# Optimization experiments

Measured on AMD Instinct MI355X. Metric: run time of the kernel, lower is better.

Reference implementation:

```python
import jax, jax.numpy as jnp
import numpy as np

N, E = 25000, 400000
NIN, NOUT, HID = 32, 32, 128


def setup_inputs() -> dict:
    key = jax.random.key(0)
    ks = jax.random.split(key, 8)
    s = lambda d: 1.0 / np.sqrt(d)
    return {
        "x": jax.random.normal(ks[0], (N, NIN), jnp.float32),
        "edge_index": jax.random.randint(ks[1], (2, E), 0, N, jnp.int64),
        "edge_attr": jax.random.normal(ks[2], (E, NIN), jnp.float32),
        # edge-MLP: Linear(NIN,HID) -> ReLU -> Linear(HID, NIN*NOUT)
        "w1": jax.random.normal(ks[3], (NIN, HID), jnp.float32) * s(NIN),
        "b1": jnp.zeros((HID,), jnp.float32),
        "w2": jax.random.normal(ks[4], (HID, NIN * NOUT), jnp.float32) * s(HID),
        "b2": jnp.zeros((NIN * NOUT,), jnp.float32),
        # NNConv root weight and bias
        "root": jax.random.normal(ks[5], (NIN, NOUT), jnp.float32) * s(NIN),
        "bias": jnp.zeros((NOUT,), jnp.float32),
    }


def reference(x, edge_index, edge_attr, w1, b1, w2, b2, root, bias):
    src, dst = edge_index[0], edge_index[1]
    # per-edge weight matrices from edge-attr MLP: [E, NIN, NOUT]
    h = jax.nn.relu(edge_attr @ w1 + b1)
    W = (h @ w2 + b2).reshape(-1, NIN, NOUT)
    # gather source features, per-edge small matmul: [E, NOUT]
    msg = jnp.einsum("ei,eio->eo", x[src], W)
    # scatter-add to target nodes (PyG default aggr='add')
    agg = jax.ops.segment_sum(msg, dst, num_segments=N)
    # root/self transform + bias
    return agg + x @ root + bias
```

## Files before the change

kernel.cpp:

```cpp
#include <hip/hip_runtime.h>
#include <hip/hip_fp16.h>


#define NN 25000
#define EE 400000

typedef _Float16 f16x8 __attribute__((ext_vector_type(8)));
typedef float    f32x16 __attribute__((ext_vector_type(16)));

__global__ __launch_bounds__(256) void prep_kernel(
    const float* __restrict__ w1, const float* __restrict__ w2,
    const float* __restrict__ b2,
    _Float16* __restrict__ w2p, _Float16* __restrict__ w1p, _Float16* __restrict__ b2p,
    float4* __restrict__ part4, int nzero4)
{
    int b = blockIdx.x;
    if (b < 532) {
        int t = b * 256 + threadIdx.x;
        if (t < 131072) {
            int j = t & 7, lane = (t >> 3) & 63, ih = (t >> 9) & 1, c = t >> 10;
            w2p[t] = (_Float16)w2[c * 1024 + (ih * 16 + ((lane >> 5) << 3) + j) * 32 + (lane & 31)];
        } else if (t < 135168) {
            int u = t - 131072;
            int j = u & 7, lane = (u >> 3) & 63, kk = (u >> 9) & 1, r = u >> 10;
            w1p[u] = (_Float16)w1[(kk * 16 + ((lane >> 5) << 3) + j) * 128 + r * 32 + (lane & 31)];
        } else {
            int u = t - 135168;
            int j = u & 7, lane = (u >> 3) & 63, ih = u >> 9;
            b2p[u] = (_Float16)b2[(ih * 16 + ((lane >> 5) << 3) + j) * 32 + (lane & 31)];
        }
    } else {
        int z = (b - 532) * 256 + threadIdx.x;
        if (z < nzero4) part4[z] = make_float4(0.f, 0.f, 0.f, 0.f);
    }
}

__global__ __launch_bounds__(256) void final_kernel(
    const float* __restrict__ x, const float* __restrict__ root,
    const float* __restrict__ bias, const float* __restrict__ part,
    int ncopies, float* __restrict__ out)
{
    int gid = blockIdx.x * 256 + threadIdx.x;
    int n = gid >> 5, o = gid & 31;
    float acc = bias[o];
    const float* xr = x + (n << 5);
#pragma unroll
    for (int i = 0; i < 32; ++i)
        acc = fmaf(xr[i], root[(i << 5) + o], acc);
    for (int c = 0; c < ncopies; ++c) acc += part[(size_t)c * 800000 + gid];
    out[gid] = acc;
}

__global__ __launch_bounds__(128, 2) void edge_kernel(
    const float*    __restrict__ x,
    const int*      __restrict__ ei,
    const float*    __restrict__ ea,
    const float*    __restrict__ b1,
    const _Float16* __restrict__ w2p,
    const _Float16* __restrict__ w1p,
    const _Float16* __restrict__ b2p,
    float* __restrict__ outp, int copyMask)
{
    __shared__ unsigned short hTq[2][32][32][4];

    const int t    = threadIdx.x;
    const int w    = t >> 6;
    const int lane = t & 63;
    const int l    = lane & 31;
    const int half = lane >> 5;

    const int  ebraw = blockIdx.x * 256 + w * 128;
    const bool live  = (ebraw + 128) <= EE;
    const int  ebw   = live ? ebraw : (EE - 128);

    float* __restrict__ myout = outp + (size_t)(blockIdx.x & copyMask) * 800000;

    union u8h { f16x8 v; __half2 h2[4]; };

    const f16x8* __restrict__ w2f = (const f16x8*)w2p;

    f16x8 BA[2], BB[2], BC[2], BD[2];
    auto loadCol = [&](int j, f16x8 (&B)[2]) {
        const f16x8* p = w2f + (size_t)j * 128 + lane;
        B[0] = p[0];
        B[1] = p[64];
    };
    loadCol(0, BA);
    loadCol(1, BB);
    loadCol(2, BC);
    loadCol(3, BD);

    u8h eaf[4][2];
#pragma unroll
    for (int g = 0; g < 4; ++g)
#pragma unroll
        for (int kk = 0; kk < 2; ++kk) {
            const float* p = ea + (size_t)(ebw + g * 32 + l) * 32 + kk * 16 + half * 8;
            float4 a0 = *(const float4*)p;
            float4 a1 = *(const float4*)(p + 4);
            eaf[g][kk].h2[0] = __float22half2_rn(make_float2(a0.x, a0.y));
            eaf[g][kk].h2[1] = __float22half2_rn(make_float2(a0.z, a0.w));
            eaf[g][kk].h2[2] = __float22half2_rn(make_float2(a1.x, a1.y));
            eaf[g][kk].h2[3] = __float22half2_rn(make_float2(a1.z, a1.w));
        }

    __half2 xs[4][8];
#pragma unroll
    for (int g = 0; g < 4; ++g) {
        int s = ei[ebw + g * 32 + l];
#pragma unroll
        for (int ih = 0; ih < 2; ++ih) {
            float4 a0 = *(const float4*)(x + s * 32 + ih * 16 + half * 8);
            float4 a1 = *(const float4*)(x + s * 32 + ih * 16 + half * 8 + 4);
            xs[g][ih*4+0] = __float22half2_rn(make_float2(a0.x, a0.y));
            xs[g][ih*4+1] = __float22half2_rn(make_float2(a0.z, a0.w));
            xs[g][ih*4+2] = __float22half2_rn(make_float2(a1.x, a1.y));
            xs[g][ih*4+3] = __float22half2_rn(make_float2(a1.z, a1.w));
        }
    }

    f32x16 acc[4];
#pragma unroll
    for (int g = 0; g < 4; ++g)
#pragma unroll
        for (int i = 0; i < 16; ++i) acc[g][i] = 0.f;

    auto phase1 = [&](int r) {
        f16x8 w1f0 = *(const f16x8*)(w1p + ((r * 2 + 0) * 64 + lane) * 8);
        f16x8 w1f1 = *(const f16x8*)(w1p + ((r * 2 + 1) * 64 + lane) * 8);
#pragma unroll
        for (int g = 0; g < 4; ++g) {
            f32x16 h;
#pragma unroll
            for (int i = 0; i < 16; ++i) h[i] = 0.f;
            h = __builtin_amdgcn_mfma_f32_32x32x16_f16(w1f0, eaf[g][0].v, h, 0, 0, 0);
            h = __builtin_amdgcn_mfma_f32_32x32x16_f16(w1f1, eaf[g][1].v, h, 0, 0, 0);
#pragma unroll
            for (int i = 0; i < 16; ++i) {
                int row = (i & 3) + ((i >> 2) << 3) + (half << 2);
                float hv = fmaxf(h[i] + b1[r * 32 + row], 0.f);
                hTq[w][row][l][g] = __half_as_ushort(__float2half(hv));
            }
        }
    };

    auto computeCol = [&](int cs, const f16x8 (&B)[2]) {
        uint2 u = *(const uint2*)&hTq[w][cs][l][0];
        __half2 ha = *reinterpret_cast<const __half2*>(&u.x);
        __half2 hb = *reinterpret_cast<const __half2*>(&u.y);
        __half2 d[4];
        d[0] = __half2half2(__low2half(ha));
        d[1] = __half2half2(__high2half(ha));
        d[2] = __half2half2(__low2half(hb));
        d[3] = __half2half2(__high2half(hb));
#pragma unroll
        for (int ih = 0; ih < 2; ++ih) {
            f16x8 bfr = B[ih];
#pragma unroll
            for (int g = 0; g < 4; ++g) {
                u8h A;
#pragma unroll
                for (int p = 0; p < 4; ++p)
                    A.h2[p] = __hmul2(d[g], xs[g][ih * 4 + p]);
                acc[g] = __builtin_amdgcn_mfma_f32_32x32x16_f16(A.v, bfr, acc[g], 0, 0, 0);
            }
        }
    };

#pragma unroll 1
    for (int r = 0; r < 4; ++r) {
        phase1(r);
#pragma unroll 1
        for (int q = 0; q < 8; ++q) {
            const int j = r * 32 + q * 4;
            computeCol(q * 4 + 0, BA); loadCol(j + 4, BA);
            computeCol(q * 4 + 1, BB); loadCol(j + 5, BB);
            computeCol(q * 4 + 2, BC); loadCol(j + 6, BC);
            computeCol(q * 4 + 3, BD); loadCol(j + 7, BD);
        }
    }

#pragma unroll
    for (int ih = 0; ih < 2; ++ih) {
        f16x8 bfr = *(const f16x8*)(b2p + (ih * 64 + lane) * 8);
#pragma unroll
        for (int g = 0; g < 4; ++g) {
            u8h A;
#pragma unroll
            for (int p = 0; p < 4; ++p) A.h2[p] = xs[g][ih * 4 + p];
            acc[g] = __builtin_amdgcn_mfma_f32_32x32x16_f16(A.v, bfr, acc[g], 0, 0, 0);
        }
    }

    if (live) {
#pragma unroll
        for (int g = 0; g < 4; ++g)
#pragma unroll
            for (int i = 0; i < 16; ++i) {
                int el = (i & 3) + ((i >> 2) << 3) + (half << 2);
                atomicAdd(myout + ei[EE + ebw + g * 32 + el] * 32 + l, acc[g][i]);
            }
    }
}

extern "C" void kernel_launch(void* const* d_in, const int* in_sizes, int n_in,
                              void* d_out, int out_size, void* d_ws, size_t ws_size,
                              hipStream_t stream) {
    const float* x    = (const float*)d_in[0];
    const int*   ei   = (const int*)  d_in[1];
    const float* ea   = (const float*)d_in[2];
    const float* w1   = (const float*)d_in[3];
    const float* b1   = (const float*)d_in[4];
    const float* w2   = (const float*)d_in[5];
    const float* b2   = (const float*)d_in[6];
    const float* root = (const float*)d_in[7];
    const float* bias = (const float*)d_in[8];
    float* out = (float*)d_out;

    _Float16* w2p = (_Float16*)d_ws;
    _Float16* w1p = (_Float16*)((char*)d_ws + 262144);
    _Float16* b2p = (_Float16*)((char*)d_ws + 270336);
    const size_t partOff = 272384;
    const size_t one = 800000ull * sizeof(float);
    size_t avail = (ws_size > partOff) ? ws_size - partOff : 0;
    int nc = 0;
    for (int c = 8; c >= 1; c >>= 1)
        if ((size_t)c * one <= avail) { nc = c; break; }

    float* part = (float*)((char*)d_ws + partOff);
    if (nc > 0) {
        int nzero4 = nc * 200000;
        int zb = (nzero4 + 255) / 256;
        prep_kernel<<<532 + zb, 256, 0, stream>>>(w1, w2, b2, w2p, w1p, b2p,
                                                  (float4*)part, nzero4);
        edge_kernel<<<(EE + 255) / 256, 128, 0, stream>>>(x, ei, ea, b1, w2p, w1p, b2p,
                                                          part, nc - 1);
        final_kernel<<<(NN * 32) / 256, 256, 0, stream>>>(x, root, bias, part, nc, out);
    } else {
        prep_kernel<<<532, 256, 0, stream>>>(w1, w2, b2, w2p, w1p, b2p, (float4*)part, 0);
        final_kernel<<<(NN * 32) / 256, 256, 0, stream>>>(x, root, bias, part, 0, out);
        edge_kernel<<<(EE + 255) / 256, 128, 0, stream>>>(x, ei, ea, b1, w2p, w1p, b2p,
                                                          out, 0);
    }
}
```

Baseline: 235.7 us.

## Replace atomic scatter with CSR build and gather-based aggregation

```diff
diff --git a/kernel.cpp b/kernel.cpp
--- a/kernel.cpp
+++ b/kernel.cpp
@@ -12,7 +12,7 @@
     const float* __restrict__ w1, const float* __restrict__ w2,
     const float* __restrict__ b2,
     _Float16* __restrict__ w2p, _Float16* __restrict__ w1p, _Float16* __restrict__ b2p,
-    float4* __restrict__ part4, int nzero4)
+    float4* __restrict__ zero4, int nzero4)
 {
     int b = blockIdx.x;
     if (b < 532) {
@@ -31,8 +31,73 @@
         }
     } else {
         int z = (b - 532) * 256 + threadIdx.x;
-        if (z < nzero4) part4[z] = make_float4(0.f, 0.f, 0.f, 0.f);
-    }
+        if (z < nzero4) zero4[z] = make_float4(0.f, 0.f, 0.f, 0.f);
+    }
+}
+
+__global__ __launch_bounds__(256) void hist_kernel(const int* __restrict__ ei,
+                                                   int* __restrict__ deg)
+{
+    int e = blockIdx.x * 256 + threadIdx.x;
+    if (e < EE) atomicAdd(&deg[ei[EE + e]], 1);
+}
+
+__global__ __launch_bounds__(1024) void scan_kernel(const int* __restrict__ deg,
+                                                    int* __restrict__ rowptr,
+                                                    int* __restrict__ cur)
+{
+    __shared__ int part[1024];
+    const int t = threadIdx.x;
+    const int base = t * 25;
+    const int cnt = (base < NN) ? ((NN - base < 25) ? (NN - base) : 25) : 0;
+    int s = 0;
+    for (int k = 0; k < cnt; ++k) s += deg[base + k];
+    part[t] = s;
+    __syncthreads();
+    for (int off = 1; off < 1024; off <<= 1) {
+        int v = (t >= off) ? part[t - off] : 0;
+        __syncthreads();
+        part[t] += v;
+        __syncthreads();
+    }
+    int excl = (t == 0) ? 0 : part[t - 1];
+    for (int k = 0; k < cnt; ++k) {
+        int d = deg[base + k];
+        rowptr[base + k] = excl;
+        cur[base + k]    = excl;
+        excl += d;
+    }
+    if (t == 1023) rowptr[NN] = part[1023];
+}
+
+__global__ __launch_bounds__(256) void fill_kernel(const int* __restrict__ ei,
+                                                   int* __restrict__ cur,
+                                                   int* __restrict__ eidx)
+{
+    int e = blockIdx.x * 256 + threadIdx.x;
+    if (e < EE) {
+        int pos = atomicAdd(&cur[ei[EE + e]], 1);
+        eidx[pos] = e;
+    }
+}
+
+__global__ __launch_bounds__(256) void final_gather(
+    const float* __restrict__ x, const float* __restrict__ root,
+    const float* __restrict__ bias, const float* __restrict__ msg,
+    const int* __restrict__ rowptr, const int* __restrict__ eidx,
+    float* __restrict__ out)
+{
+    int gid = blockIdx.x * 256 + threadIdx.x;
+    int n = gid >> 5, o = gid & 31;
+    float acc = bias[o];
+    const float* xr = x + (n << 5);
+#pragma unroll
+    for (int i = 0; i < 32; ++i)
+        acc = fmaf(xr[i], root[(i << 5) + o], acc);
+    int k0 = rowptr[n], k1 = rowptr[n + 1];
+    for (int k = k0; k < k1; ++k)
+        acc += msg[(size_t)eidx[k] * 32 + o];
+    out[gid] = acc;
 }
 
 __global__ __launch_bounds__(256) void final_kernel(
@@ -59,7 +124,7 @@
     const _Float16* __restrict__ w2p,
     const _Float16* __restrict__ w1p,
     const _Float16* __restrict__ b2p,
-    float* __restrict__ outp, int copyMask)
+    float* __restrict__ outp, int copyMask, int useStore)
 {
     __shared__ unsigned short hTq[2][32][32][4];
 
@@ -193,13 +258,23 @@
     }
 
     if (live) {
-#pragma unroll
-        for (int g = 0; g < 4; ++g)
-#pragma unroll
-            for (int i = 0; i < 16; ++i) {
-                int el = (i & 3) + ((i >> 2) << 3) + (half << 2);
-                atomicAdd(myout + ei[EE + ebw + g * 32 + el] * 32 + l, acc[g][i]);
-            }
+        if (useStore) {
+#pragma unroll
+            for (int g = 0; g < 4; ++g)
+#pragma unroll
+                for (int i = 0; i < 16; ++i) {
+                    int el = (i & 3) + ((i >> 2) << 3) + (half << 2);
+                    myout[(size_t)(ebw + g * 32 + el) * 32 + l] = acc[g][i];
+                }
+        } else {
+#pragma unroll
+            for (int g = 0; g < 4; ++g)
+#pragma unroll
+                for (int i = 0; i < 16; ++i) {
+                    int el = (i & 3) + ((i >> 2) << 3) + (half << 2);
+                    atomicAdd(myout + ei[EE + ebw + g * 32 + el] * 32 + l, acc[g][i]);
+                }
+        }
     }
 }
 
@@ -220,6 +295,35 @@
     _Float16* w2p = (_Float16*)d_ws;
     _Float16* w1p = (_Float16*)((char*)d_ws + 262144);
     _Float16* b2p = (_Float16*)((char*)d_ws + 270336);
+
+    const size_t degOff  = 272384;
+    const size_t rowOff  = 372384;
+    const size_t curOff  = 472400;
+    const size_t eidxOff = 572400;
+    const size_t msgOff  = 2172400;
+    const size_t needStore = msgOff + (size_t)EE * 32 * 4;
+
+    if (ws_size >= needStore) {
+        int*   deg    = (int*)((char*)d_ws + degOff);
+        int*   rowptr = (int*)((char*)d_ws + rowOff);
+        int*   cur    = (int*)((char*)d_ws + curOff);
+        int*   eidx   = (int*)((char*)d_ws + eidxOff);
+        float* msg    = (float*)((char*)d_ws + msgOff);
+
+        int nzero4 = 25000 / 4;
+        int zb = (nzero4 + 255) / 256;
+        prep_kernel<<<532 + zb, 256, 0, stream>>>(w1, w2, b2, w2p, w1p, b2p,
+                                                  (float4*)deg, nzero4);
+        hist_kernel<<<(EE + 255) / 256, 256, 0, stream>>>(ei, deg);
+        scan_kernel<<<1, 1024, 0, stream>>>(deg, rowptr, cur);
+        fill_kernel<<<(EE + 255) / 256, 256, 0, stream>>>(ei, cur, eidx);
+        edge_kernel<<<(EE + 255) / 256, 128, 0, stream>>>(x, ei, ea, b1, w2p, w1p, b2p,
+                                                          msg, 0, 1);
+        final_gather<<<(NN * 32) / 256, 256, 0, stream>>>(x, root, bias, msg,
+                                                          rowptr, eidx, out);
+        return;
+    }
+
     const size_t partOff = 272384;
     const size_t one = 800000ull * sizeof(float);
     size_t avail = (ws_size > partOff) ? ws_size - partOff : 0;
@@ -234,12 +338,12 @@
         prep_kernel<<<532 + zb, 256, 0, stream>>>(w1, w2, b2, w2p, w1p, b2p,
                                                   (float4*)part, nzero4);
         edge_kernel<<<(EE + 255) / 256, 128, 0, stream>>>(x, ei, ea, b1, w2p, w1p, b2p,
-                                                          part, nc - 1);
+                                                          part, nc - 1, 0);
         final_kernel<<<(NN * 32) / 256, 256, 0, stream>>>(x, root, bias, part, nc, out);
     } else {
         prep_kernel<<<532, 256, 0, stream>>>(w1, w2, b2, w2p, w1p, b2p, (float4*)part, 0);
         final_kernel<<<(NN * 32) / 256, 256, 0, stream>>>(x, root, bias, part, 0, out);
         edge_kernel<<<(EE + 255) / 256, 128, 0, stream>>>(x, ei, ea, b1, w2p, w1p, b2p,
-                                                          out, 0);
-    }
-}
+                                                          out, 0, 0);
+    }
+}
```

After: 327.8 us. 39.1% more time.

## Fuse prep, root transform and edge kernel into one cooperative grid-synced kernel

Applied to the files above, without the earlier changes.

```diff
diff --git a/kernel.cpp b/kernel.cpp
--- a/kernel.cpp
+++ b/kernel.cpp
@@ -1,18 +1,22 @@
 #include <hip/hip_runtime.h>
 #include <hip/hip_fp16.h>
+#include <hip/hip_cooperative_groups.h>
 
 
 #define NN 25000
 #define EE 400000
 
+namespace cg = cooperative_groups;
+
 typedef _Float16 f16x8 __attribute__((ext_vector_type(8)));
 typedef float    f32x16 __attribute__((ext_vector_type(16)));
+
 
 __global__ __launch_bounds__(256) void prep_kernel(
     const float* __restrict__ w1, const float* __restrict__ w2,
     const float* __restrict__ b2,
     _Float16* __restrict__ w2p, _Float16* __restrict__ w1p, _Float16* __restrict__ b2p,
-    float4* __restrict__ part4, int nzero4)
+    float4* __restrict__ zero4, int nzero4)
 {
     int b = blockIdx.x;
     if (b < 532) {
@@ -31,7 +35,7 @@
         }
     } else {
         int z = (b - 532) * 256 + threadIdx.x;
-        if (z < nzero4) part4[z] = make_float4(0.f, 0.f, 0.f, 0.f);
+        if (z < nzero4) zero4[z] = make_float4(0.f, 0.f, 0.f, 0.f);
     }
 }
 
@@ -85,10 +89,7 @@
         B[0] = p[0];
         B[1] = p[64];
     };
-    loadCol(0, BA);
-    loadCol(1, BB);
-    loadCol(2, BC);
-    loadCol(3, BD);
+    loadCol(0, BA); loadCol(1, BB); loadCol(2, BC); loadCol(3, BD);
 
     u8h eaf[4][2];
 #pragma unroll
@@ -199,6 +200,187 @@
             for (int i = 0; i < 16; ++i) {
                 int el = (i & 3) + ((i >> 2) << 3) + (half << 2);
                 atomicAdd(myout + ei[EE + ebw + g * 32 + el] * 32 + l, acc[g][i]);
+            }
+    }
+}
+
+__global__ __launch_bounds__(128, 4) void fused_kernel(
+    const float*    __restrict__ x,
+    const int*      __restrict__ ei,
+    const float*    __restrict__ ea,
+    const float*    __restrict__ w1,
+    const float*    __restrict__ b1,
+    const float*    __restrict__ w2,
+    const float*    __restrict__ b2,
+    const float*    __restrict__ root,
+    const float*    __restrict__ bias,
+    _Float16*       __restrict__ w2p,
+    _Float16*       __restrict__ w1p,
+    _Float16*       __restrict__ b2p,
+    float*          __restrict__ out)
+{
+    __shared__ unsigned short hTq[2][32][32][4];
+
+    const int tid    = blockIdx.x * 128 + threadIdx.x;
+    const int stride = gridDim.x * 128;
+
+    for (int t = tid; t < 136192; t += stride) {
+        if (t < 131072) {
+            int j = t & 7, lane = (t >> 3) & 63, ih = (t >> 9) & 1, c = t >> 10;
+            w2p[t] = (_Float16)w2[c * 1024 + (ih * 16 + ((lane >> 5) << 3) + j) * 32 + (lane & 31)];
+        } else if (t < 135168) {
+            int u = t - 131072;
+            int j = u & 7, lane = (u >> 3) & 63, kk = (u >> 9) & 1, r = u >> 10;
+            w1p[u] = (_Float16)w1[(kk * 16 + ((lane >> 5) << 3) + j) * 128 + r * 32 + (lane & 31)];
+        } else {
+            int u = t - 135168;
+            int j = u & 7, lane = (u >> 3) & 63, ih = u >> 9;
+            b2p[u] = (_Float16)b2[(ih * 16 + ((lane >> 5) << 3) + j) * 32 + (lane & 31)];
+        }
+    }
+    for (int gidx = tid; gidx < NN * 32; gidx += stride) {
+        int n = gidx >> 5, o = gidx & 31;
+        float a = bias[o];
+        const float* xr = x + (n << 5);
+#pragma unroll
+        for (int i = 0; i < 32; ++i)
+            a = fmaf(xr[i], root[(i << 5) + o], a);
+        out[gidx] = a;
+    }
+
+    cg::this_grid().sync();
+
+    const int t    = threadIdx.x;
+    const int w    = t >> 6;
+    const int lane = t & 63;
+    const int l    = lane & 31;
+    const int half = lane >> 5;
+
+    const int  ebraw = blockIdx.x * 256 + w * 128;
+    const bool live  = (ebraw + 128) <= EE;
+    const int  ebw   = live ? ebraw : (EE - 128);
+
+    union u8h { f16x8 v; __half2 h2[4]; };
+
+    const f16x8* __restrict__ w2f = (const f16x8*)w2p;
+
+    f16x8 BA[2], BB[2], BC[2], BD[2];
+    auto loadCol = [&](int j, f16x8 (&B)[2]) {
+        const f16x8* p = w2f + (size_t)j * 128 + lane;
+        B[0] = p[0];
+        B[1] = p[64];
+    };
+    loadCol(0, BA); loadCol(1, BB); loadCol(2, BC); loadCol(3, BD);
+
+    u8h eaf[4][2];
+#pragma unroll
+    for (int g = 0; g < 4; ++g)
+#pragma unroll
+        for (int kk = 0; kk < 2; ++kk) {
+            const float* p = ea + (size_t)(ebw + g * 32 + l) * 32 + kk * 16 + half * 8;
+            float4 a0 = *(const float4*)p;
+            float4 a1 = *(const float4*)(p + 4);
+            eaf[g][kk].h2[0] = __float22half2_rn(make_float2(a0.x, a0.y));
+            eaf[g][kk].h2[1] = __float22half2_rn(make_float2(a0.z, a0.w));
+            eaf[g][kk].h2[2] = __float22half2_rn(make_float2(a1.x, a1.y));
+            eaf[g][kk].h2[3] = __float22half2_rn(make_float2(a1.z, a1.w));
+        }
+
+    __half2 xs[4][8];
+#pragma unroll
+    for (int g = 0; g < 4; ++g) {
+        int s = ei[ebw + g * 32 + l];
+#pragma unroll
+        for (int ih = 0; ih < 2; ++ih) {
+            float4 a0 = *(const float4*)(x + s * 32 + ih * 16 + half * 8);
+            float4 a1 = *(const float4*)(x + s * 32 + ih * 16 + half * 8 + 4);
+            xs[g][ih*4+0] = __float22half2_rn(make_float2(a0.x, a0.y));
+            xs[g][ih*4+1] = __float22half2_rn(make_float2(a0.z, a0.w));
+            xs[g][ih*4+2] = __float22half2_rn(make_float2(a1.x, a1.y));
+            xs[g][ih*4+3] = __float22half2_rn(make_float2(a1.z, a1.w));
+        }
+    }
+
+    f32x16 acc[4];
+#pragma unroll
+    for (int g = 0; g < 4; ++g)
+#pragma unroll
+        for (int i = 0; i < 16; ++i) acc[g][i] = 0.f;
+
+    auto phase1 = [&](int r) {
+        f16x8 w1f0 = *(const f16x8*)(w1p + ((r * 2 + 0) * 64 + lane) * 8);
+        f16x8 w1f1 = *(const f16x8*)(w1p + ((r * 2 + 1) * 64 + lane) * 8);
+#pragma unroll
+        for (int g = 0; g < 4; ++g) {
+            f32x16 h;
+#pragma unroll
+            for (int i = 0; i < 16; ++i) h[i] = 0.f;
+            h = __builtin_amdgcn_mfma_f32_32x32x16_f16(w1f0, eaf[g][0].v, h, 0, 0, 0);
+            h = __builtin_amdgcn_mfma_f32_32x32x16_f16(w1f1, eaf[g][1].v, h, 0, 0, 0);
+#pragma unroll
+            for (int i = 0; i < 16; ++i) {
+                int row = (i & 3) + ((i >> 2) << 3) + (half << 2);
+                float hv = fmaxf(h[i] + b1[r * 32 + row], 0.f);
+                hTq[w][row][l][g] = __half_as_ushort(__float2half(hv));
+            }
+        }
+    };
+
+    auto computeCol = [&](int cs, const f16x8 (&B)[2]) {
+        uint2 u = *(const uint2*)&hTq[w][cs][l][0];
+        __half2 ha = *reinterpret_cast<const __half2*>(&u.x);
+        __half2 hb = *reinterpret_cast<const __half2*>(&u.y);
+        __half2 d[4];
+        d[0] = __half2half2(__low2half(ha));
+        d[1] = __half2half2(__high2half(ha));
+        d[2] = __half2half2(__low2half(hb));
+        d[3] = __half2half2(__high2half(hb));
+#pragma unroll
+        for (int ih = 0; ih < 2; ++ih) {
+            f16x8 bfr = B[ih];
+#pragma unroll
+            for (int g = 0; g < 4; ++g) {
+                u8h A;
+#pragma unroll
+                for (int p = 0; p < 4; ++p)
+                    A.h2[p] = __hmul2(d[g], xs[g][ih * 4 + p]);
+                acc[g] = __builtin_amdgcn_mfma_f32_32x32x16_f16(A.v, bfr, acc[g], 0, 0, 0);
+            }
+        }
+    };
+
+#pragma unroll 1
+    for (int r = 0; r < 4; ++r) {
+        phase1(r);
+#pragma unroll 1
+        for (int q = 0; q < 8; ++q) {
+            const int j = r * 32 + q * 4;
+            computeCol(q * 4 + 0, BA); loadCol(j + 4, BA);
+            computeCol(q * 4 + 1, BB); loadCol(j + 5, BB);
+            computeCol(q * 4 + 2, BC); loadCol(j + 6, BC);
+            computeCol(q * 4 + 3, BD); loadCol(j + 7, BD);
+        }
+    }
+
+#pragma unroll
+    for (int ih = 0; ih < 2; ++ih) {
+        f16x8 bfr = *(const f16x8*)(b2p + (ih * 64 + lane) * 8);
+#pragma unroll
+        for (int g = 0; g < 4; ++g) {
+            u8h A;
+#pragma unroll
+            for (int p = 0; p < 4; ++p) A.h2[p] = xs[g][ih * 4 + p];
+            acc[g] = __builtin_amdgcn_mfma_f32_32x32x16_f16(A.v, bfr, acc[g], 0, 0, 0);
+        }
+    }
+
+    if (live) {
+#pragma unroll
+        for (int g = 0; g < 4; ++g)
+#pragma unroll
+            for (int i = 0; i < 16; ++i) {
+                int el = (i & 3) + ((i >> 2) << 3) + (half << 2);
+                atomicAdd(out + (size_t)ei[EE + ebw + g * 32 + el] * 32 + l, acc[g][i]);
             }
     }
 }
@@ -220,6 +402,23 @@
     _Float16* w2p = (_Float16*)d_ws;
     _Float16* w1p = (_Float16*)((char*)d_ws + 262144);
     _Float16* b2p = (_Float16*)((char*)d_ws + 270336);
+
+    const int GRID = (EE + 255) / 256;
+    int nb = 0;
+    hipError_t qe = hipOccupancyMaxActiveBlocksPerMultiprocessor(&nb, fused_kernel, 128, 0);
+    bool launched = false;
+    if (qe == hipSuccess && nb * 256 >= GRID) {
+        void* args[] = {
+            (void*)&x, (void*)&ei, (void*)&ea, (void*)&w1, (void*)&b1,
+            (void*)&w2, (void*)&b2, (void*)&root, (void*)&bias,
+            (void*)&w2p, (void*)&w1p, (void*)&b2p, (void*)&out
+        };
+        hipError_t le = hipLaunchCooperativeKernel(
+            (const void*)fused_kernel, dim3(GRID), dim3(128), args, 0, stream);
+        launched = (le == hipSuccess);
+    }
+    if (launched) return;
+
     const size_t partOff = 272384;
     const size_t one = 800000ull * sizeof(float);
     size_t avail = (ws_size > partOff) ? ws_size - partOff : 0;
@@ -233,13 +432,13 @@
         int zb = (nzero4 + 255) / 256;
         prep_kernel<<<532 + zb, 256, 0, stream>>>(w1, w2, b2, w2p, w1p, b2p,
                                                   (float4*)part, nzero4);
-        edge_kernel<<<(EE + 255) / 256, 128, 0, stream>>>(x, ei, ea, b1, w2p, w1p, b2p,
-                                                          part, nc - 1);
+        edge_kernel<<<GRID, 128, 0, stream>>>(x, ei, ea, b1, w2p, w1p, b2p,
+                                              part, nc - 1);
         final_kernel<<<(NN * 32) / 256, 256, 0, stream>>>(x, root, bias, part, nc, out);
     } else {
         prep_kernel<<<532, 256, 0, stream>>>(w1, w2, b2, w2p, w1p, b2p, (float4*)part, 0);
         final_kernel<<<(NN * 32) / 256, 256, 0, stream>>>(x, root, bias, part, 0, out);
-        edge_kernel<<<(EE + 255) / 256, 128, 0, stream>>>(x, ei, ea, b1, w2p, w1p, b2p,
-                                                          out, 0);
+        edge_kernel<<<GRID, 128, 0, stream>>>(x, ei, ea, b1, w2p, w1p, b2p,
+                                              out, 0);
     }
 }
```

After: 235.4 us. No clear change (-0.1%).

## Fuse prep and root transform, drop replicated partial buffers for direct atomics

Applied to the files above, without the earlier changes.

```diff
diff --git a/kernel.cpp b/kernel.cpp
--- a/kernel.cpp
+++ b/kernel.cpp
@@ -8,47 +8,36 @@
 typedef _Float16 f16x8 __attribute__((ext_vector_type(8)));
 typedef float    f32x16 __attribute__((ext_vector_type(16)));
 
-__global__ __launch_bounds__(256) void prep_kernel(
+__global__ __launch_bounds__(256) void prep_final_kernel(
+    const float* __restrict__ x, const float* __restrict__ root,
+    const float* __restrict__ bias,
     const float* __restrict__ w1, const float* __restrict__ w2,
     const float* __restrict__ b2,
     _Float16* __restrict__ w2p, _Float16* __restrict__ w1p, _Float16* __restrict__ b2p,
-    float4* __restrict__ part4, int nzero4)
+    float* __restrict__ out)
 {
-    int b = blockIdx.x;
-    if (b < 532) {
-        int t = b * 256 + threadIdx.x;
-        if (t < 131072) {
-            int j = t & 7, lane = (t >> 3) & 63, ih = (t >> 9) & 1, c = t >> 10;
-            w2p[t] = (_Float16)w2[c * 1024 + (ih * 16 + ((lane >> 5) << 3) + j) * 32 + (lane & 31)];
-        } else if (t < 135168) {
-            int u = t - 131072;
-            int j = u & 7, lane = (u >> 3) & 63, kk = (u >> 9) & 1, r = u >> 10;
-            w1p[u] = (_Float16)w1[(kk * 16 + ((lane >> 5) << 3) + j) * 128 + r * 32 + (lane & 31)];
-        } else {
-            int u = t - 135168;
-            int j = u & 7, lane = (u >> 3) & 63, ih = u >> 9;
-            b2p[u] = (_Float16)b2[(ih * 16 + ((lane >> 5) << 3) + j) * 32 + (lane & 31)];
-        }
-    } else {
-        int z = (b - 532) * 256 + threadIdx.x;
-        if (z < nzero4) part4[z] = make_float4(0.f, 0.f, 0.f, 0.f);
-    }
-}
-
-__global__ __launch_bounds__(256) void final_kernel(
-    const float* __restrict__ x, const float* __restrict__ root,
-    const float* __restrict__ bias, const float* __restrict__ part,
-    int ncopies, float* __restrict__ out)
-{
-    int gid = blockIdx.x * 256 + threadIdx.x;
-    int n = gid >> 5, o = gid & 31;
+    const int t = blockIdx.x * 256 + threadIdx.x;
+
+    if (t < 131072) {
+        int j = t & 7, lane = (t >> 3) & 63, ih = (t >> 9) & 1, c = t >> 10;
+        w2p[t] = (_Float16)w2[c * 1024 + (ih * 16 + ((lane >> 5) << 3) + j) * 32 + (lane & 31)];
+    } else if (t < 135168) {
+        int u = t - 131072;
+        int j = u & 7, lane = (u >> 3) & 63, kk = (u >> 9) & 1, r = u >> 10;
+        w1p[u] = (_Float16)w1[(kk * 16 + ((lane >> 5) << 3) + j) * 128 + r * 32 + (lane & 31)];
+    } else if (t < 136192) {
+        int u = t - 135168;
+        int j = u & 7, lane = (u >> 3) & 63, ih = u >> 9;
+        b2p[u] = (_Float16)b2[(ih * 16 + ((lane >> 5) << 3) + j) * 32 + (lane & 31)];
+    }
+
+    int n = t >> 5, o = t & 31;
     float acc = bias[o];
     const float* xr = x + (n << 5);
 #pragma unroll
     for (int i = 0; i < 32; ++i)
         acc = fmaf(xr[i], root[(i << 5) + o], acc);
-    for (int c = 0; c < ncopies; ++c) acc += part[(size_t)c * 800000 + gid];
-    out[gid] = acc;
+    out[t] = acc;
 }
 
 __global__ __launch_bounds__(128, 2) void edge_kernel(
@@ -59,7 +48,7 @@
     const _Float16* __restrict__ w2p,
     const _Float16* __restrict__ w1p,
     const _Float16* __restrict__ b2p,
-    float* __restrict__ outp, int copyMask)
+    float* __restrict__ out)
 {
     __shared__ unsigned short hTq[2][32][32][4];
 
@@ -72,8 +61,6 @@
     const int  ebraw = blockIdx.x * 256 + w * 128;
     const bool live  = (ebraw + 128) <= EE;
     const int  ebw   = live ? ebraw : (EE - 128);
-
-    float* __restrict__ myout = outp + (size_t)(blockIdx.x & copyMask) * 800000;
 
     union u8h { f16x8 v; __half2 h2[4]; };
 
@@ -85,10 +72,7 @@
         B[0] = p[0];
         B[1] = p[64];
     };
-    loadCol(0, BA);
-    loadCol(1, BB);
-    loadCol(2, BC);
-    loadCol(3, BD);
+    loadCol(0, BA); loadCol(1, BB); loadCol(2, BC); loadCol(3, BD);
 
     u8h eaf[4][2];
 #pragma unroll
@@ -198,7 +182,7 @@
 #pragma unroll
             for (int i = 0; i < 16; ++i) {
                 int el = (i & 3) + ((i >> 2) << 3) + (half << 2);
-                atomicAdd(myout + ei[EE + ebw + g * 32 + el] * 32 + l, acc[g][i]);
+                atomicAdd(out + (size_t)ei[EE + ebw + g * 32 + el] * 32 + l, acc[g][i]);
             }
     }
 }
@@ -220,26 +204,10 @@
     _Float16* w2p = (_Float16*)d_ws;
     _Float16* w1p = (_Float16*)((char*)d_ws + 262144);
     _Float16* b2p = (_Float16*)((char*)d_ws + 270336);
-    const size_t partOff = 272384;
-    const size_t one = 800000ull * sizeof(float);
-    size_t avail = (ws_size > partOff) ? ws_size - partOff : 0;
-    int nc = 0;
-    for (int c = 8; c >= 1; c >>= 1)
-        if ((size_t)c * one <= avail) { nc = c; break; }
-
-    float* part = (float*)((char*)d_ws + partOff);
-    if (nc > 0) {
-        int nzero4 = nc * 200000;
-        int zb = (nzero4 + 255) / 256;
-        prep_kernel<<<532 + zb, 256, 0, stream>>>(w1, w2, b2, w2p, w1p, b2p,
-                                                  (float4*)part, nzero4);
-        edge_kernel<<<(EE + 255) / 256, 128, 0, stream>>>(x, ei, ea, b1, w2p, w1p, b2p,
-                                                          part, nc - 1);
-        final_kernel<<<(NN * 32) / 256, 256, 0, stream>>>(x, root, bias, part, nc, out);
-    } else {
-        prep_kernel<<<532, 256, 0, stream>>>(w1, w2, b2, w2p, w1p, b2p, (float4*)part, 0);
-        final_kernel<<<(NN * 32) / 256, 256, 0, stream>>>(x, root, bias, part, 0, out);
-        edge_kernel<<<(EE + 255) / 256, 128, 0, stream>>>(x, ei, ea, b1, w2p, w1p, b2p,
-                                                          out, 0);
-    }
+
+    prep_final_kernel<<<(NN * 32) / 256, 256, 0, stream>>>(
+        x, root, bias, w1, w2, b2, w2p, w1p, b2p, out);
+
+    edge_kernel<<<(EE + 255) / 256, 128, 0, stream>>>(
+        x, ei, ea, b1, w2p, w1p, b2p, out);
 }
```

Measured after the change: 225.5 us. 4.3% less time.
